# Kernel optimization log

Hardware: AMD Instinct MI355X
Metric: run time of the kernel (lower is better)

## Reference

```python
import jax, jax.numpy as jnp
import numpy as np
import math

N_HEAD = 16
N_KV_HEAD = 4
WINDOW = 512
EPS = 1e-6


def _rotate_half(t):
    t1, t2 = jnp.split(t, 2, axis=-1)
    return jnp.concatenate([-t2, t1], axis=-1)


def _rope_tables(T, head_dim):
    theta = 1.0 / (10000.0 ** (jnp.arange(0, head_dim, 2, dtype=jnp.float32) / head_dim))
    pos = jnp.arange(T, dtype=jnp.float32)
    freqs = jnp.outer(pos, theta)                      # [T, d/2]
    cos = jnp.concatenate([jnp.cos(freqs), jnp.cos(freqs)], axis=-1)  # [T, d]
    sin = jnp.concatenate([jnp.sin(freqs), jnp.sin(freqs)], axis=-1)
    return cos, sin


def setup_inputs() -> dict:
    key = jax.random.key(0)
    k1, k2, k3, k4 = jax.random.split(key, 4)
    B, T, C = 1, 2048, 1024
    kv_out = 2 * N_KV_HEAD * (C // N_HEAD)  # 512
    x = jax.random.normal(k1, (B, T, C), dtype=jnp.float32)
    Wq = jax.random.normal(k2, (C, C), dtype=jnp.float32) * 0.02
    Wkv = jax.random.normal(k3, (kv_out, C), dtype=jnp.float32) * 0.02
    Wproj = jax.random.normal(k4, (C, C), dtype=jnp.float32) * 0.02
    return {"x": x, "Wq": Wq, "Wkv": Wkv, "Wproj": Wproj}


def reference(x, Wq, Wkv, Wproj):
    B, T, C = x.shape
    H, KV = N_HEAD, N_KV_HEAD
    d = C // H
    n_rep = H // KV

    q = (x @ Wq.T).reshape(B, T, H, d).transpose(0, 2, 1, 3)     # [B,H,T,d]
    kv = x @ Wkv.T                                               # [B,T,2*KV*d]
    k, v = jnp.split(kv, 2, axis=2)
    k = k.reshape(B, T, KV, d).transpose(0, 2, 1, 3)             # [B,KV,T,d]
    v = v.reshape(B, T, KV, d).transpose(0, 2, 1, 3)

    # QK L2 normalization
    q = q / (jnp.linalg.norm(q, axis=-1, keepdims=True) + EPS)
    k = k / (jnp.linalg.norm(k, axis=-1, keepdims=True) + EPS)

    # RoPE
    cos, sin = _rope_tables(T, d)
    cos = cos[None, None]  # [1,1,T,d]
    sin = sin[None, None]
    q = q * cos + _rotate_half(q) * sin
    k = k * cos + _rotate_half(k) * sin

    # GQA: repeat KV heads (repeat_interleave on head dim)
    k = jnp.repeat(k, n_rep, axis=1)   # [B,H,T,d]
    v = jnp.repeat(v, n_rep, axis=1)

    # sliding-window causal mask: cols <= rows and cols > rows - WINDOW
    rows = jnp.arange(T)[:, None]
    cols = jnp.arange(T)[None, :]
    mask = (cols <= rows) & (cols > rows - WINDOW)  # [T,T] bool

    scale = 1.0 / math.sqrt(d)
    scores = jnp.einsum("bhqd,bhkd->bhqk", q, k) * scale
    scores = jnp.where(mask[None, None], scores, -jnp.inf)
    attn = jax.nn.softmax(scores, axis=-1)
    y = jnp.einsum("bhqk,bhkd->bhqd", attn, v)      # [B,H,T,d]
    y = y.transpose(0, 2, 1, 3).reshape(B, T, C)
    return y @ Wproj.T
```

## Files before the change

kernel.cpp:

```cpp
#include <hip/hip_runtime.h>

#define T_SEQ 2048
#define C_DIM 1024
#define NH    16
#define NKV   4
#define HD    64
#define WIN   512

typedef __bf16 bf16x8 __attribute__((ext_vector_type(8)));
typedef __bf16 bf16x4 __attribute__((ext_vector_type(4)));
typedef float f32x4 __attribute__((ext_vector_type(4)));

#define MFMA16(a, b, c) __builtin_amdgcn_mfma_f32_16x16x32_bf16(a, b, c, 0, 0, 0)

__global__ __launch_bounds__(256) void prep_kernel(const float* __restrict__ x,
                                                   const float* __restrict__ Wq,
                                                   const float* __restrict__ Wkv,
                                                   const float* __restrict__ Wp,
                                                   __bf16* __restrict__ xb,
                                                   __bf16* __restrict__ Wqkvb,
                                                   __bf16* __restrict__ Wpb,
                                                   float2* __restrict__ ropeT) {
  int b = blockIdx.x;
  if (b >= 4608) {
    int idx = (b - 4608) * 256 + threadIdx.x;
    int t = idx >> 5, i = idx & 31;
    float theta = exp2f(-(float)i * (13.287712379549449f / 32.0f));
    float s, c;
    sincosf((float)t * theta, &s, &c);
    ropeT[idx] = make_float2(c, s);
    return;
  }
  const float* src;
  __bf16* dst;
  int off;
  if (b < 2048)      { src = x;   dst = xb;                off = b; }
  else if (b < 3072) { src = Wq;  dst = Wqkvb;             off = b - 2048; }
  else if (b < 3584) { src = Wkv; dst = Wqkvb + (1 << 20); off = b - 3072; }
  else               { src = Wp;  dst = Wpb;               off = b - 3584; }
  int i = off * 1024 + threadIdx.x * 4;
  float4 v = *(const float4*)(src + i);
  bf16x4 o;
  o[0] = (__bf16)v.x; o[1] = (__bf16)v.y; o[2] = (__bf16)v.z; o[3] = (__bf16)v.w;
  *(bf16x4*)(dst + i) = o;
}

__device__ __forceinline__ void gemm_core64(const __bf16* __restrict__ A,
                                            const __bf16* __restrict__ B,
                                            int K,
                                            __bf16* AsB, __bf16* BsB,
                                            f32x4 (&acc)[4]) {
  const int tid = threadIdx.x;
  const int w = tid >> 6, l = tid & 63;
  const int quad = l >> 4, r16 = l & 15;
  const int srow = tid >> 2;
  const int sc0  = (tid & 3) * 2;
  const int wS0 = srow * 64 + ((sc0 ^ (srow & 7)) * 8);
  const int wS1 = srow * 64 + (((sc0 + 1) ^ (srow & 7)) * 8);
  const __bf16* gA = A + (size_t)srow * K + sc0 * 8;
  const __bf16* gB = B + (size_t)srow * K + sc0 * 8;
  int rA[2], rB[4][2];
#pragma unroll
  for (int ks = 0; ks < 2; ++ks) {
    int row = w * 16 + r16;
    rA[ks] = row * 64 + (((ks * 4 + quad) ^ (row & 7)) * 8);
  }
#pragma unroll
  for (int nt = 0; nt < 4; ++nt)
#pragma unroll
    for (int ks = 0; ks < 2; ++ks) {
      int row = nt * 16 + r16;
      rB[nt][ks] = row * 64 + (((ks * 4 + quad) ^ (row & 7)) * 8);
    }
  const int nIter = K >> 6;
  uint4 a0, a1, b0, b1;
  { const uint4* p = (const uint4*)gA; a0 = p[0]; a1 = p[1]; }
  { const uint4* p = (const uint4*)gB; b0 = p[0]; b1 = p[1]; }
  *(uint4*)(AsB + wS0) = a0; *(uint4*)(AsB + wS1) = a1;
  *(uint4*)(BsB + wS0) = b0; *(uint4*)(BsB + wS1) = b1;
  __syncthreads();
  int cur = 0;
  for (int it = 0; it < nIter; ++it) {
    if (it + 1 < nIter) {
      const uint4* p = (const uint4*)(gA + ((it + 1) << 6));
      a0 = p[0]; a1 = p[1];
      const uint4* q = (const uint4*)(gB + ((it + 1) << 6));
      b0 = q[0]; b1 = q[1];
    }
    const __bf16* Asc = AsB + cur * 4096;
    const __bf16* Bsc = BsB + cur * 4096;
#pragma unroll
    for (int ks = 0; ks < 2; ++ks) {
      bf16x8 fa  = *(const bf16x8*)(Asc + rA[ks]);
      bf16x8 fb0 = *(const bf16x8*)(Bsc + rB[0][ks]);
      bf16x8 fb1 = *(const bf16x8*)(Bsc + rB[1][ks]);
      bf16x8 fb2 = *(const bf16x8*)(Bsc + rB[2][ks]);
      bf16x8 fb3 = *(const bf16x8*)(Bsc + rB[3][ks]);
      acc[0] = MFMA16(fa, fb0, acc[0]);
      acc[1] = MFMA16(fa, fb1, acc[1]);
      acc[2] = MFMA16(fa, fb2, acc[2]);
      acc[3] = MFMA16(fa, fb3, acc[3]);
    }
    if (it + 1 < nIter) {
      __builtin_amdgcn_sched_barrier(0);
      __bf16* Asn = AsB + (cur ^ 1) * 4096;
      __bf16* Bsn = BsB + (cur ^ 1) * 4096;
      *(uint4*)(Asn + wS0) = a0; *(uint4*)(Asn + wS1) = a1;
      *(uint4*)(Bsn + wS0) = b0; *(uint4*)(Bsn + wS1) = b1;
      __syncthreads();
      cur ^= 1;
    }
  }
}

__global__ __launch_bounds__(256) void gemm_qkv_kernel(const __bf16* __restrict__ xb,
                                                       const __bf16* __restrict__ Wqkvb,
                                                       const float2* __restrict__ ropeT,
                                                       __bf16* __restrict__ Qb,
                                                       __bf16* __restrict__ Kb,
                                                       __bf16* __restrict__ Vt) {
  __shared__ __align__(16) __bf16 smem[16384];
  __bf16* AsB = smem;
  __bf16* BsB = smem + 8192;
  f32x4 acc[4] = {};
  const int m0 = blockIdx.y * 64, n0 = blockIdx.x * 64;
  gemm_core64(xb + (size_t)m0 * C_DIM, Wqkvb + (size_t)n0 * C_DIM, C_DIM, AsB, BsB, acc);
  const int tid = threadIdx.x;
  const int w = tid >> 6, l = tid & 63, quad = l >> 4, r16 = l & 15;
  if (n0 < 1280) {
    const bool isQ = n0 < 1024;
    const int head = isQ ? (n0 >> 6) : ((n0 - 1024) >> 6);
    __bf16* dstBase = (isQ ? Qb : Kb) + (size_t)head * T_SEQ * HD;
    const float osc = isQ ? 0.125f : 1.0f;
#pragma unroll
    for (int r = 0; r < 4; ++r) {
      float ss = acc[0][r] * acc[0][r] + acc[1][r] * acc[1][r] +
                 acc[2][r] * acc[2][r] + acc[3][r] * acc[3][r];
#pragma unroll
      for (int m = 1; m < 16; m <<= 1) ss += __shfl_xor(ss, m, 64);
      const float inv = osc / (sqrtf(ss) + 1e-6f);
      const int t = m0 + w * 16 + quad * 4 + r;
      const float2 cs0 = ropeT[t * 32 + r16];
      const float2 cs1 = ropeT[t * 32 + 16 + r16];
      const float v0 = acc[0][r] * inv, v1 = acc[1][r] * inv;
      const float v2 = acc[2][r] * inv, v3 = acc[3][r] * inv;
      __bf16* dst = dstBase + (size_t)t * HD;
      dst[r16]      = (__bf16)(v0 * cs0.x - v2 * cs0.y);
      dst[16 + r16] = (__bf16)(v1 * cs1.x - v3 * cs1.y);
      dst[32 + r16] = (__bf16)(v2 * cs0.x + v0 * cs0.y);
      dst[48 + r16] = (__bf16)(v3 * cs1.x + v1 * cs1.y);
    }
  } else {
    const int kvh = (n0 - 1280) >> 6;
    __syncthreads();
    __bf16* Vs = smem;
#pragma unroll
    for (int nt = 0; nt < 4; ++nt)
#pragma unroll
      for (int r = 0; r < 4; ++r)
        Vs[(nt * 16 + r16) * 136 + w * 16 + quad * 4 + r] = (__bf16)acc[nt][r];
    __syncthreads();
    const int d = tid >> 2, tc = (tid & 3) * 16;
    __bf16* dst = Vt + ((size_t)kvh * HD + d) * T_SEQ + m0 + tc;
    bf16x8 v0 = *(const bf16x8*)(Vs + d * 136 + tc);
    bf16x8 v1 = *(const bf16x8*)(Vs + d * 136 + tc + 8);
    *(bf16x8*)dst = v0;
    *(bf16x8*)(dst + 8) = v1;
  }
}

__global__ __launch_bounds__(256) void gemm_proj_kernel(const __bf16* __restrict__ Yb,
                                                        const __bf16* __restrict__ Wpb,
                                                        float* __restrict__ C) {
  __shared__ __align__(16) __bf16 smem[16384];
  __bf16* AsB = smem;
  __bf16* BsB = smem + 8192;
  f32x4 acc[4] = {};
  const int m0 = blockIdx.y * 64, n0 = blockIdx.x * 64;
  gemm_core64(Yb + (size_t)m0 * C_DIM, Wpb + (size_t)n0 * C_DIM, C_DIM, AsB, BsB, acc);
  const int tid = threadIdx.x;
  const int w = tid >> 6, l = tid & 63, quad = l >> 4, r16 = l & 15;
  const int mrow = m0 + w * 16 + quad * 4;
  const int ncol = n0 + r16;
#pragma unroll
  for (int r = 0; r < 4; ++r) {
    size_t rowoff = (size_t)(mrow + r) * C_DIM;
    C[rowoff + ncol]      = acc[0][r];
    C[rowoff + ncol + 16] = acc[1][r];
    C[rowoff + ncol + 32] = acc[2][r];
    C[rowoff + ncol + 48] = acc[3][r];
  }
}

__global__ __launch_bounds__(256) void attn_mfma_kernel(const __bf16* __restrict__ Qb,
                                                        const __bf16* __restrict__ Kb,
                                                        const __bf16* __restrict__ Vt,
                                                        __bf16* __restrict__ Yb) {
  __shared__ __align__(16) __bf16 Pl[4][16][72];
  __shared__ __align__(16) float Oc[2][16][68];
  __shared__ float Ls[2][16];
  const int h = blockIdx.y, kvh = h >> 2;
  const int t0 = blockIdx.x * 32;
  const int tid = threadIdx.x;
  const int w = tid >> 6, l = tid & 63;
  const int quad = l >> 4, r16 = l & 15;
  const int sub = w & 1, half = w >> 1;
  const __bf16* qptr = Qb + ((size_t)h * T_SEQ + t0 + sub * 16 + r16) * HD + quad * 8;
  bf16x8 aq0 = *(const bf16x8*)(qptr);
  bf16x8 aq1 = *(const bf16x8*)(qptr + 32);
  const int keyStart = max(0, t0 - (WIN - 1)) & ~63;
  const int keyEnd = (t0 + 32 + 63) & ~63;
  const int nch = (keyEnd - keyStart) >> 6;
  const int nch2 = (nch + 1) >> 1;
  const int cbeg = half ? nch2 : 0;
  const int cend = half ? nch : nch2;
  const __bf16* kbase = Kb + (size_t)kvh * T_SEQ * HD;
  const __bf16* vbase = Vt + (size_t)kvh * HD * T_SEQ;
  const int tq_base = t0 + sub * 16 + quad * 4;
  f32x4 oacc[4] = {};
  float lsum[4] = {0.f, 0.f, 0.f, 0.f};
  for (int c = cbeg; c < cend; ++c) {
    const int key0 = keyStart + (c << 6);
    f32x4 s[4] = {};
#pragma unroll
    for (int nt = 0; nt < 4; ++nt) {
      const __bf16* kr = kbase + (size_t)(key0 + nt * 16 + r16) * HD + quad * 8;
      bf16x8 bk0 = *(const bf16x8*)kr;
      bf16x8 bk1 = *(const bf16x8*)(kr + 32);
      s[nt] = MFMA16(aq0, bk0, s[nt]);
      s[nt] = MFMA16(aq1, bk1, s[nt]);
    }
#pragma unroll
    for (int nt = 0; nt < 4; ++nt) {
      const int key = key0 + nt * 16 + r16;
#pragma unroll
      for (int r = 0; r < 4; ++r) {
        const int tq = tq_base + r;
        bool valid = (key <= tq) && (key > tq - WIN);
        float p = valid ? __expf(s[nt][r]) : 0.0f;
        lsum[r] += p;
        Pl[w][quad * 4 + r][nt * 16 + r16] = (__bf16)p;
      }
    }
    bf16x8 ap0 = *(const bf16x8*)(&Pl[w][r16][quad * 8]);
    bf16x8 ap1 = *(const bf16x8*)(&Pl[w][r16][32 + quad * 8]);
#pragma unroll
    for (int nt = 0; nt < 4; ++nt) {
      const __bf16* vr = vbase + (size_t)(nt * 16 + r16) * T_SEQ + key0 + quad * 8;
      bf16x8 bv0 = *(const bf16x8*)vr;
      bf16x8 bv1 = *(const bf16x8*)(vr + 32);
      oacc[nt] = MFMA16(ap0, bv0, oacc[nt]);
      oacc[nt] = MFMA16(ap1, bv1, oacc[nt]);
    }
  }
#pragma unroll
  for (int r = 0; r < 4; ++r) {
#pragma unroll
    for (int m = 1; m < 16; m <<= 1) lsum[r] += __shfl_xor(lsum[r], m, 64);
  }
  if (half == 1) {
#pragma unroll
    for (int nt = 0; nt < 4; ++nt)
#pragma unroll
      for (int r = 0; r < 4; ++r)
        Oc[sub][quad * 4 + r][nt * 16 + r16] = oacc[nt][r];
    if (r16 == 0) {
#pragma unroll
      for (int r = 0; r < 4; ++r) Ls[sub][quad * 4 + r] = lsum[r];
    }
  }
  __syncthreads();
  if (half == 0) {
#pragma unroll
    for (int r = 0; r < 4; ++r) {
      const float inv = 1.0f / (lsum[r] + Ls[sub][quad * 4 + r]);
      const size_t row = (size_t)(tq_base + r);
#pragma unroll
      for (int nt = 0; nt < 4; ++nt) {
        float o = oacc[nt][r] + Oc[sub][quad * 4 + r][nt * 16 + r16];
        Yb[row * C_DIM + h * HD + nt * 16 + r16] = (__bf16)(o * inv);
      }
    }
  }
}

extern "C" void kernel_launch(void* const* d_in, const int* in_sizes, int n_in,
                              void* d_out, int out_size, void* d_ws, size_t ws_size,
                              hipStream_t stream) {
  const float* x     = (const float*)d_in[0];
  const float* Wq    = (const float*)d_in[1];
  const float* Wkv   = (const float*)d_in[2];
  const float* Wproj = (const float*)d_in[3];
  float* out = (float*)d_out;

  __bf16* xb    = (__bf16*)d_ws;
  __bf16* Wqkvb = xb + (size_t)T_SEQ * C_DIM;
  __bf16* Wpb   = Wqkvb + (size_t)1536 * C_DIM;
  __bf16* Qb    = Wpb + (size_t)C_DIM * C_DIM;
  __bf16* Kb    = Qb + (size_t)NH * T_SEQ * HD;
  __bf16* Vt    = Kb + (size_t)NKV * T_SEQ * HD;
  __bf16* Yb    = Vt + (size_t)NKV * HD * T_SEQ;
  float2* ropeT = (float2*)(Yb + (size_t)T_SEQ * C_DIM);

  prep_kernel<<<4864, 256, 0, stream>>>(x, Wq, Wkv, Wproj, xb, Wqkvb, Wpb, ropeT);
  gemm_qkv_kernel<<<dim3(24, 32), 256, 0, stream>>>(xb, Wqkvb, ropeT, Qb, Kb, Vt);
  attn_mfma_kernel<<<dim3(T_SEQ / 32, NH), 256, 0, stream>>>(Qb, Kb, Vt, Yb);
  gemm_proj_kernel<<<dim3(16, 32), 256, 0, stream>>>(Yb, Wpb, out);
}
```

Baseline: 133.1 us.

## Split K across two thread groups in both GEMMs with shared-memory reduction

Both GEMM kernels now launch 512 threads per block. Each 256-thread half computes the 64x64 tile over half of the K dimension, using its own double-buffered shared-memory region. The second half writes its partial accumulators to shared memory and the first half adds them before the epilogue. This aims to double the waves per tile and improve latency hiding for small grids (768 and 512 blocks). The cost is twice the shared memory per block, an extra reduction round, and idle threads during the epilogue.

New measurement: 135.4 us. About the same (+1.7%).

```diff
diff --git a/kernel.cpp b/kernel.cpp
--- a/kernel.cpp
+++ b/kernel.cpp
@@ -45,20 +45,25 @@
   *(bf16x4*)(dst + i) = o;
 }
 
-__device__ __forceinline__ void gemm_core64(const __bf16* __restrict__ A,
-                                            const __bf16* __restrict__ B,
-                                            int K,
-                                            __bf16* AsB, __bf16* BsB,
-                                            f32x4 (&acc)[4]) {
-  const int tid = threadIdx.x;
+__device__ __forceinline__ void gemm_core_sk(const __bf16* __restrict__ A,
+                                             const __bf16* __restrict__ B,
+                                             int K,
+                                             __bf16* smem,
+                                             f32x4 (&acc)[4]) {
+  const int tid512 = threadIdx.x;
+  const int g = tid512 >> 8;
+  const int tid = tid512 & 255;
   const int w = tid >> 6, l = tid & 63;
   const int quad = l >> 4, r16 = l & 15;
   const int srow = tid >> 2;
   const int sc0  = (tid & 3) * 2;
   const int wS0 = srow * 64 + ((sc0 ^ (srow & 7)) * 8);
   const int wS1 = srow * 64 + (((sc0 + 1) ^ (srow & 7)) * 8);
-  const __bf16* gA = A + (size_t)srow * K + sc0 * 8;
-  const __bf16* gB = B + (size_t)srow * K + sc0 * 8;
+  const int kOff = g * (K >> 1);
+  const __bf16* gA = A + (size_t)srow * K + kOff + sc0 * 8;
+  const __bf16* gB = B + (size_t)srow * K + kOff + sc0 * 8;
+  __bf16* AsB = smem + g * 16384;
+  __bf16* BsB = smem + g * 16384 + 8192;
   int rA[2], rB[4][2];
 #pragma unroll
   for (int ks = 0; ks < 2; ++ks) {
@@ -72,7 +77,7 @@
       int row = nt * 16 + r16;
       rB[nt][ks] = row * 64 + (((ks * 4 + quad) ^ (row & 7)) * 8);
     }
-  const int nIter = K >> 6;
+  const int nIter = (K >> 1) >> 6;
   uint4 a0, a1, b0, b1;
   { const uint4* p = (const uint4*)gA; a0 = p[0]; a1 = p[1]; }
   { const uint4* p = (const uint4*)gB; b0 = p[0]; b1 = p[1]; }
@@ -111,74 +116,95 @@
       cur ^= 1;
     }
   }
-}
-
-__global__ __launch_bounds__(256) void gemm_qkv_kernel(const __bf16* __restrict__ xb,
-                                                       const __bf16* __restrict__ Wqkvb,
-                                                       const float2* __restrict__ ropeT,
-                                                       __bf16* __restrict__ Qb,
-                                                       __bf16* __restrict__ Kb,
-                                                       __bf16* __restrict__ Vt) {
-  __shared__ __align__(16) __bf16 smem[16384];
-  __bf16* AsB = smem;
-  __bf16* BsB = smem + 8192;
+  __syncthreads();
+  float* Sc = (float*)smem;
+  if (g == 1) {
+#pragma unroll
+    for (int nt = 0; nt < 4; ++nt)
+      *(f32x4*)(Sc + (nt * 16 + r16) * 68 + (w * 16 + quad * 4)) = acc[nt];
+  }
+  __syncthreads();
+  if (g == 0) {
+#pragma unroll
+    for (int nt = 0; nt < 4; ++nt) {
+      f32x4 o = *(const f32x4*)(Sc + (nt * 16 + r16) * 68 + (w * 16 + quad * 4));
+      acc[nt] = acc[nt] + o;
+    }
+  }
+}
+
+__global__ __launch_bounds__(512, 4) void gemm_qkv_kernel(const __bf16* __restrict__ xb,
+                                                          const __bf16* __restrict__ Wqkvb,
+                                                          const float2* __restrict__ ropeT,
+                                                          __bf16* __restrict__ Qb,
+                                                          __bf16* __restrict__ Kb,
+                                                          __bf16* __restrict__ Vt) {
+  __shared__ __align__(16) __bf16 smem[32768];
   f32x4 acc[4] = {};
   const int m0 = blockIdx.y * 64, n0 = blockIdx.x * 64;
-  gemm_core64(xb + (size_t)m0 * C_DIM, Wqkvb + (size_t)n0 * C_DIM, C_DIM, AsB, BsB, acc);
-  const int tid = threadIdx.x;
+  gemm_core_sk(xb + (size_t)m0 * C_DIM, Wqkvb + (size_t)n0 * C_DIM, C_DIM, smem, acc);
+  const int tid512 = threadIdx.x;
+  const int g = tid512 >> 8;
+  const int tid = tid512 & 255;
   const int w = tid >> 6, l = tid & 63, quad = l >> 4, r16 = l & 15;
   if (n0 < 1280) {
-    const bool isQ = n0 < 1024;
-    const int head = isQ ? (n0 >> 6) : ((n0 - 1024) >> 6);
-    __bf16* dstBase = (isQ ? Qb : Kb) + (size_t)head * T_SEQ * HD;
-    const float osc = isQ ? 0.125f : 1.0f;
-#pragma unroll
-    for (int r = 0; r < 4; ++r) {
-      float ss = acc[0][r] * acc[0][r] + acc[1][r] * acc[1][r] +
-                 acc[2][r] * acc[2][r] + acc[3][r] * acc[3][r];
-#pragma unroll
-      for (int m = 1; m < 16; m <<= 1) ss += __shfl_xor(ss, m, 64);
-      const float inv = osc / (sqrtf(ss) + 1e-6f);
-      const int t = m0 + w * 16 + quad * 4 + r;
-      const float2 cs0 = ropeT[t * 32 + r16];
-      const float2 cs1 = ropeT[t * 32 + 16 + r16];
-      const float v0 = acc[0][r] * inv, v1 = acc[1][r] * inv;
-      const float v2 = acc[2][r] * inv, v3 = acc[3][r] * inv;
-      __bf16* dst = dstBase + (size_t)t * HD;
-      dst[r16]      = (__bf16)(v0 * cs0.x - v2 * cs0.y);
-      dst[16 + r16] = (__bf16)(v1 * cs1.x - v3 * cs1.y);
-      dst[32 + r16] = (__bf16)(v2 * cs0.x + v0 * cs0.y);
-      dst[48 + r16] = (__bf16)(v3 * cs1.x + v1 * cs1.y);
+    if (g == 0) {
+      const bool isQ = n0 < 1024;
+      const int head = isQ ? (n0 >> 6) : ((n0 - 1024) >> 6);
+      __bf16* dstBase = (isQ ? Qb : Kb) + (size_t)head * T_SEQ * HD;
+      const float osc = isQ ? 0.125f : 1.0f;
+#pragma unroll
+      for (int r = 0; r < 4; ++r) {
+        float ss = acc[0][r] * acc[0][r] + acc[1][r] * acc[1][r] +
+                   acc[2][r] * acc[2][r] + acc[3][r] * acc[3][r];
+#pragma unroll
+        for (int m = 1; m < 16; m <<= 1) ss += __shfl_xor(ss, m, 64);
+        const float inv = osc / (sqrtf(ss) + 1e-6f);
+        const int t = m0 + w * 16 + quad * 4 + r;
+        const float2 cs0 = ropeT[t * 32 + r16];
+        const float2 cs1 = ropeT[t * 32 + 16 + r16];
+        const float v0 = acc[0][r] * inv, v1 = acc[1][r] * inv;
+        const float v2 = acc[2][r] * inv, v3 = acc[3][r] * inv;
+        __bf16* dst = dstBase + (size_t)t * HD;
+        dst[r16]      = (__bf16)(v0 * cs0.x - v2 * cs0.y);
+        dst[16 + r16] = (__bf16)(v1 * cs1.x - v3 * cs1.y);
+        dst[32 + r16] = (__bf16)(v2 * cs0.x + v0 * cs0.y);
+        dst[48 + r16] = (__bf16)(v3 * cs1.x + v1 * cs1.y);
+      }
     }
   } else {
     const int kvh = (n0 - 1280) >> 6;
     __syncthreads();
     __bf16* Vs = smem;
-#pragma unroll
-    for (int nt = 0; nt < 4; ++nt)
-#pragma unroll
-      for (int r = 0; r < 4; ++r)
-        Vs[(nt * 16 + r16) * 136 + w * 16 + quad * 4 + r] = (__bf16)acc[nt][r];
+    if (g == 0) {
+#pragma unroll
+      for (int nt = 0; nt < 4; ++nt)
+#pragma unroll
+        for (int r = 0; r < 4; ++r)
+          Vs[(nt * 16 + r16) * 136 + w * 16 + quad * 4 + r] = (__bf16)acc[nt][r];
+    }
     __syncthreads();
-    const int d = tid >> 2, tc = (tid & 3) * 16;
-    __bf16* dst = Vt + ((size_t)kvh * HD + d) * T_SEQ + m0 + tc;
-    bf16x8 v0 = *(const bf16x8*)(Vs + d * 136 + tc);
-    bf16x8 v1 = *(const bf16x8*)(Vs + d * 136 + tc + 8);
-    *(bf16x8*)dst = v0;
-    *(bf16x8*)(dst + 8) = v1;
-  }
-}
-
-__global__ __launch_bounds__(256) void gemm_proj_kernel(const __bf16* __restrict__ Yb,
-                                                        const __bf16* __restrict__ Wpb,
-                                                        float* __restrict__ C) {
-  __shared__ __align__(16) __bf16 smem[16384];
-  __bf16* AsB = smem;
-  __bf16* BsB = smem + 8192;
+    if (g == 0) {
+      const int d = tid >> 2, tc = (tid & 3) * 16;
+      __bf16* dst = Vt + ((size_t)kvh * HD + d) * T_SEQ + m0 + tc;
+      bf16x8 v0 = *(const bf16x8*)(Vs + d * 136 + tc);
+      bf16x8 v1 = *(const bf16x8*)(Vs + d * 136 + tc + 8);
+      *(bf16x8*)dst = v0;
+      *(bf16x8*)(dst + 8) = v1;
+    }
+  }
+}
+
+__global__ __launch_bounds__(512, 4) void gemm_proj_kernel(const __bf16* __restrict__ Yb,
+                                                           const __bf16* __restrict__ Wpb,
+                                                           float* __restrict__ C) {
+  __shared__ __align__(16) __bf16 smem[32768];
   f32x4 acc[4] = {};
   const int m0 = blockIdx.y * 64, n0 = blockIdx.x * 64;
-  gemm_core64(Yb + (size_t)m0 * C_DIM, Wpb + (size_t)n0 * C_DIM, C_DIM, AsB, BsB, acc);
-  const int tid = threadIdx.x;
+  gemm_core_sk(Yb + (size_t)m0 * C_DIM, Wpb + (size_t)n0 * C_DIM, C_DIM, smem, acc);
+  const int tid512 = threadIdx.x;
+  if (tid512 >= 256) return;
+  const int tid = tid512;
   const int w = tid >> 6, l = tid & 63, quad = l >> 4, r16 = l & 15;
   const int mrow = m0 + w * 16 + quad * 4;
   const int ncol = n0 + r16;
@@ -303,7 +329,7 @@
   float2* ropeT = (float2*)(Yb + (size_t)T_SEQ * C_DIM);
 
   prep_kernel<<<4864, 256, 0, stream>>>(x, Wq, Wkv, Wproj, xb, Wqkvb, Wpb, ropeT);
-  gemm_qkv_kernel<<<dim3(24, 32), 256, 0, stream>>>(xb, Wqkvb, ropeT, Qb, Kb, Vt);
+  gemm_qkv_kernel<<<dim3(24, 32), 512, 0, stream>>>(xb, Wqkvb, ropeT, Qb, Kb, Vt);
   attn_mfma_kernel<<<dim3(T_SEQ / 32, NH), 256, 0, stream>>>(Qb, Kb, Vt, Yb);
-  gemm_proj_kernel<<<dim3(16, 32), 256, 0, stream>>>(Yb, Wpb, out);
-}
+  gemm_proj_kernel<<<dim3(16, 32), 512, 0, stream>>>(Yb, Wpb, out);
+}
```

## Fuse all four stages into one persistent kernel with grid barriers

Applied to the files above, without the earlier changes.

Replaces the four separate launches (prep, QKV GEMM, attention, projection GEMM) with a single persistent kernel of 1024 blocks that runs each stage in turn, separated by atomic-counter grid barriers. The barrier counters are cleared with a memset before launch. The aim is to remove the launch gaps and tail effects between kernels. In exchange, the spin-wait barriers cost time, some blocks sit idle in the GEMM stages, and the scheme only works if all 1024 blocks are resident at once (launch_bounds 256,4). If they are not, it deadlocks.

Result: slower. 468.0 us (+251.6%).

```diff
diff --git a/kernel.cpp b/kernel.cpp
--- a/kernel.cpp
+++ b/kernel.cpp
@@ -6,6 +6,7 @@
 #define NKV   4
 #define HD    64
 #define WIN   512
+#define NBLK  1024u
 
 typedef __bf16 bf16x8 __attribute__((ext_vector_type(8)));
 typedef __bf16 bf16x4 __attribute__((ext_vector_type(4)));
@@ -13,36 +14,15 @@
 
 #define MFMA16(a, b, c) __builtin_amdgcn_mfma_f32_16x16x32_bf16(a, b, c, 0, 0, 0)
 
-__global__ __launch_bounds__(256) void prep_kernel(const float* __restrict__ x,
-                                                   const float* __restrict__ Wq,
-                                                   const float* __restrict__ Wkv,
-                                                   const float* __restrict__ Wp,
-                                                   __bf16* __restrict__ xb,
-                                                   __bf16* __restrict__ Wqkvb,
-                                                   __bf16* __restrict__ Wpb,
-                                                   float2* __restrict__ ropeT) {
-  int b = blockIdx.x;
-  if (b >= 4608) {
-    int idx = (b - 4608) * 256 + threadIdx.x;
-    int t = idx >> 5, i = idx & 31;
-    float theta = exp2f(-(float)i * (13.287712379549449f / 32.0f));
-    float s, c;
-    sincosf((float)t * theta, &s, &c);
-    ropeT[idx] = make_float2(c, s);
-    return;
-  }
-  const float* src;
-  __bf16* dst;
-  int off;
-  if (b < 2048)      { src = x;   dst = xb;                off = b; }
-  else if (b < 3072) { src = Wq;  dst = Wqkvb;             off = b - 2048; }
-  else if (b < 3584) { src = Wkv; dst = Wqkvb + (1 << 20); off = b - 3072; }
-  else               { src = Wp;  dst = Wpb;               off = b - 3584; }
-  int i = off * 1024 + threadIdx.x * 4;
-  float4 v = *(const float4*)(src + i);
-  bf16x4 o;
-  o[0] = (__bf16)v.x; o[1] = (__bf16)v.y; o[2] = (__bf16)v.z; o[3] = (__bf16)v.w;
-  *(bf16x4*)(dst + i) = o;
+__device__ __forceinline__ void grid_barrier(unsigned* cnt) {
+  __syncthreads();
+  if (threadIdx.x == 0) {
+    __threadfence();
+    atomicAdd(cnt, 1u);
+    while (atomicAdd(cnt, 0u) < NBLK) __builtin_amdgcn_s_sleep(8);
+    __threadfence();
+  }
+  __syncthreads();
 }
 
 __device__ __forceinline__ void gemm_core64(const __bf16* __restrict__ A,
@@ -113,173 +93,199 @@
   }
 }
 
-__global__ __launch_bounds__(256) void gemm_qkv_kernel(const __bf16* __restrict__ xb,
-                                                       const __bf16* __restrict__ Wqkvb,
-                                                       const float2* __restrict__ ropeT,
+__global__ __launch_bounds__(256, 4) void fused_kernel(const float* __restrict__ x,
+                                                       const float* __restrict__ Wq,
+                                                       const float* __restrict__ Wkv,
+                                                       const float* __restrict__ Wp,
+                                                       __bf16* __restrict__ xb,
+                                                       __bf16* __restrict__ Wqkvb,
+                                                       __bf16* __restrict__ Wpb,
+                                                       float2* __restrict__ ropeT,
                                                        __bf16* __restrict__ Qb,
                                                        __bf16* __restrict__ Kb,
-                                                       __bf16* __restrict__ Vt) {
+                                                       __bf16* __restrict__ Vt,
+                                                       __bf16* __restrict__ Yb,
+                                                       float* __restrict__ out,
+                                                       unsigned* __restrict__ bar) {
   __shared__ __align__(16) __bf16 smem[16384];
-  __bf16* AsB = smem;
-  __bf16* BsB = smem + 8192;
-  f32x4 acc[4] = {};
-  const int m0 = blockIdx.y * 64, n0 = blockIdx.x * 64;
-  gemm_core64(xb + (size_t)m0 * C_DIM, Wqkvb + (size_t)n0 * C_DIM, C_DIM, AsB, BsB, acc);
+  const int bid = blockIdx.x;
   const int tid = threadIdx.x;
   const int w = tid >> 6, l = tid & 63, quad = l >> 4, r16 = l & 15;
-  if (n0 < 1280) {
-    const bool isQ = n0 < 1024;
-    const int head = isQ ? (n0 >> 6) : ((n0 - 1024) >> 6);
-    __bf16* dstBase = (isQ ? Qb : Kb) + (size_t)head * T_SEQ * HD;
-    const float osc = isQ ? 0.125f : 1.0f;
+
+  for (int b = bid; b < 4864; b += (int)NBLK) {
+    if (b >= 4608) {
+      int idx = (b - 4608) * 256 + tid;
+      int t = idx >> 5, i = idx & 31;
+      float theta = exp2f(-(float)i * (13.287712379549449f / 32.0f));
+      float s, c;
+      sincosf((float)t * theta, &s, &c);
+      ropeT[idx] = make_float2(c, s);
+    } else {
+      const float* src;
+      __bf16* dst;
+      int off;
+      if (b < 2048)      { src = x;   dst = xb;                off = b; }
+      else if (b < 3072) { src = Wq;  dst = Wqkvb;             off = b - 2048; }
+      else if (b < 3584) { src = Wkv; dst = Wqkvb + (1 << 20); off = b - 3072; }
+      else               { src = Wp;  dst = Wpb;               off = b - 3584; }
+      int i = off * 1024 + tid * 4;
+      float4 v = *(const float4*)(src + i);
+      bf16x4 o;
+      o[0] = (__bf16)v.x; o[1] = (__bf16)v.y; o[2] = (__bf16)v.z; o[3] = (__bf16)v.w;
+      *(bf16x4*)(dst + i) = o;
+    }
+  }
+  grid_barrier(bar + 0);
+
+  if (bid < 768) {
+    f32x4 acc[4] = {};
+    const int m0 = (bid / 24) * 64, n0 = (bid % 24) * 64;
+    gemm_core64(xb + (size_t)m0 * C_DIM, Wqkvb + (size_t)n0 * C_DIM, C_DIM,
+                smem, smem + 8192, acc);
+    if (n0 < 1280) {
+      const bool isQ = n0 < 1024;
+      const int head = isQ ? (n0 >> 6) : ((n0 - 1024) >> 6);
+      __bf16* dstBase = (isQ ? Qb : Kb) + (size_t)head * T_SEQ * HD;
+      const float osc = isQ ? 0.125f : 1.0f;
+#pragma unroll
+      for (int r = 0; r < 4; ++r) {
+        float ss = acc[0][r] * acc[0][r] + acc[1][r] * acc[1][r] +
+                   acc[2][r] * acc[2][r] + acc[3][r] * acc[3][r];
+#pragma unroll
+        for (int m = 1; m < 16; m <<= 1) ss += __shfl_xor(ss, m, 64);
+        const float inv = osc / (sqrtf(ss) + 1e-6f);
+        const int t = m0 + w * 16 + quad * 4 + r;
+        const float2 cs0 = ropeT[t * 32 + r16];
+        const float2 cs1 = ropeT[t * 32 + 16 + r16];
+        const float v0 = acc[0][r] * inv, v1 = acc[1][r] * inv;
+        const float v2 = acc[2][r] * inv, v3 = acc[3][r] * inv;
+        __bf16* dst = dstBase + (size_t)t * HD;
+        dst[r16]      = (__bf16)(v0 * cs0.x - v2 * cs0.y);
+        dst[16 + r16] = (__bf16)(v1 * cs1.x - v3 * cs1.y);
+        dst[32 + r16] = (__bf16)(v2 * cs0.x + v0 * cs0.y);
+        dst[48 + r16] = (__bf16)(v3 * cs1.x + v1 * cs1.y);
+      }
+    } else {
+      const int kvh = (n0 - 1280) >> 6;
+      __syncthreads();
+      __bf16* Vs = smem;
+#pragma unroll
+      for (int nt = 0; nt < 4; ++nt)
+#pragma unroll
+        for (int r = 0; r < 4; ++r)
+          Vs[(nt * 16 + r16) * 136 + w * 16 + quad * 4 + r] = (__bf16)acc[nt][r];
+      __syncthreads();
+      const int d = tid >> 2, tc = (tid & 3) * 16;
+      __bf16* dst = Vt + ((size_t)kvh * HD + d) * T_SEQ + m0 + tc;
+      bf16x8 v0 = *(const bf16x8*)(Vs + d * 136 + tc);
+      bf16x8 v1 = *(const bf16x8*)(Vs + d * 136 + tc + 8);
+      *(bf16x8*)dst = v0;
+      *(bf16x8*)(dst + 8) = v1;
+    }
+  }
+  grid_barrier(bar + 1);
+
+  {
+    __bf16* Pl = smem;
+    float*  Oc = (float*)(smem + 4608);
+    float*  Ls = Oc + 2176;
+    const int h = bid >> 6, kvh = h >> 2;
+    const int t0 = (bid & 63) * 32;
+    const int sub = w & 1, half = w >> 1;
+    const __bf16* qptr = Qb + ((size_t)h * T_SEQ + t0 + sub * 16 + r16) * HD + quad * 8;
+    bf16x8 aq0 = *(const bf16x8*)(qptr);
+    bf16x8 aq1 = *(const bf16x8*)(qptr + 32);
+    const int keyStart = max(0, t0 - (WIN - 1)) & ~63;
+    const int keyEnd = (t0 + 32 + 63) & ~63;
+    const int nch = (keyEnd - keyStart) >> 6;
+    const int nch2 = (nch + 1) >> 1;
+    const int cbeg = half ? nch2 : 0;
+    const int cend = half ? nch : nch2;
+    const __bf16* kbase = Kb + (size_t)kvh * T_SEQ * HD;
+    const __bf16* vbase = Vt + (size_t)kvh * HD * T_SEQ;
+    const int tq_base = t0 + sub * 16 + quad * 4;
+    f32x4 oacc[4] = {};
+    float lsum[4] = {0.f, 0.f, 0.f, 0.f};
+    for (int c = cbeg; c < cend; ++c) {
+      const int key0 = keyStart + (c << 6);
+      f32x4 s[4] = {};
+#pragma unroll
+      for (int nt = 0; nt < 4; ++nt) {
+        const __bf16* kr = kbase + (size_t)(key0 + nt * 16 + r16) * HD + quad * 8;
+        bf16x8 bk0 = *(const bf16x8*)kr;
+        bf16x8 bk1 = *(const bf16x8*)(kr + 32);
+        s[nt] = MFMA16(aq0, bk0, s[nt]);
+        s[nt] = MFMA16(aq1, bk1, s[nt]);
+      }
+#pragma unroll
+      for (int nt = 0; nt < 4; ++nt) {
+        const int key = key0 + nt * 16 + r16;
+#pragma unroll
+        for (int r = 0; r < 4; ++r) {
+          const int tq = tq_base + r;
+          bool valid = (key <= tq) && (key > tq - WIN);
+          float p = valid ? __expf(s[nt][r]) : 0.0f;
+          lsum[r] += p;
+          Pl[(w * 16 + quad * 4 + r) * 72 + nt * 16 + r16] = (__bf16)p;
+        }
+      }
+      bf16x8 ap0 = *(const bf16x8*)(Pl + (w * 16 + r16) * 72 + quad * 8);
+      bf16x8 ap1 = *(const bf16x8*)(Pl + (w * 16 + r16) * 72 + 32 + quad * 8);
+#pragma unroll
+      for (int nt = 0; nt < 4; ++nt) {
+        const __bf16* vr = vbase + (size_t)(nt * 16 + r16) * T_SEQ + key0 + quad * 8;
+        bf16x8 bv0 = *(const bf16x8*)vr;
+        bf16x8 bv1 = *(const bf16x8*)(vr + 32);
+        oacc[nt] = MFMA16(ap0, bv0, oacc[nt]);
+        oacc[nt] = MFMA16(ap1, bv1, oacc[nt]);
+      }
+    }
 #pragma unroll
     for (int r = 0; r < 4; ++r) {
-      float ss = acc[0][r] * acc[0][r] + acc[1][r] * acc[1][r] +
-                 acc[2][r] * acc[2][r] + acc[3][r] * acc[3][r];
-#pragma unroll
-      for (int m = 1; m < 16; m <<= 1) ss += __shfl_xor(ss, m, 64);
-      const float inv = osc / (sqrtf(ss) + 1e-6f);
-      const int t = m0 + w * 16 + quad * 4 + r;
-      const float2 cs0 = ropeT[t * 32 + r16];
-      const float2 cs1 = ropeT[t * 32 + 16 + r16];
-      const float v0 = acc[0][r] * inv, v1 = acc[1][r] * inv;
-      const float v2 = acc[2][r] * inv, v3 = acc[3][r] * inv;
-      __bf16* dst = dstBase + (size_t)t * HD;
-      dst[r16]      = (__bf16)(v0 * cs0.x - v2 * cs0.y);
-      dst[16 + r16] = (__bf16)(v1 * cs1.x - v3 * cs1.y);
-      dst[32 + r16] = (__bf16)(v2 * cs0.x + v0 * cs0.y);
-      dst[48 + r16] = (__bf16)(v3 * cs1.x + v1 * cs1.y);
-    }
-  } else {
-    const int kvh = (n0 - 1280) >> 6;
+#pragma unroll
+      for (int m = 1; m < 16; m <<= 1) lsum[r] += __shfl_xor(lsum[r], m, 64);
+    }
+    if (half == 1) {
+#pragma unroll
+      for (int nt = 0; nt < 4; ++nt)
+#pragma unroll
+        for (int r = 0; r < 4; ++r)
+          Oc[(sub * 16 + quad * 4 + r) * 68 + nt * 16 + r16] = oacc[nt][r];
+      if (r16 == 0) {
+#pragma unroll
+        for (int r = 0; r < 4; ++r) Ls[sub * 16 + quad * 4 + r] = lsum[r];
+      }
+    }
     __syncthreads();
-    __bf16* Vs = smem;
-#pragma unroll
-    for (int nt = 0; nt < 4; ++nt)
-#pragma unroll
-      for (int r = 0; r < 4; ++r)
-        Vs[(nt * 16 + r16) * 136 + w * 16 + quad * 4 + r] = (__bf16)acc[nt][r];
-    __syncthreads();
-    const int d = tid >> 2, tc = (tid & 3) * 16;
-    __bf16* dst = Vt + ((size_t)kvh * HD + d) * T_SEQ + m0 + tc;
-    bf16x8 v0 = *(const bf16x8*)(Vs + d * 136 + tc);
-    bf16x8 v1 = *(const bf16x8*)(Vs + d * 136 + tc + 8);
-    *(bf16x8*)dst = v0;
-    *(bf16x8*)(dst + 8) = v1;
-  }
-}
-
-__global__ __launch_bounds__(256) void gemm_proj_kernel(const __bf16* __restrict__ Yb,
-                                                        const __bf16* __restrict__ Wpb,
-                                                        float* __restrict__ C) {
-  __shared__ __align__(16) __bf16 smem[16384];
-  __bf16* AsB = smem;
-  __bf16* BsB = smem + 8192;
-  f32x4 acc[4] = {};
-  const int m0 = blockIdx.y * 64, n0 = blockIdx.x * 64;
-  gemm_core64(Yb + (size_t)m0 * C_DIM, Wpb + (size_t)n0 * C_DIM, C_DIM, AsB, BsB, acc);
-  const int tid = threadIdx.x;
-  const int w = tid >> 6, l = tid & 63, quad = l >> 4, r16 = l & 15;
-  const int mrow = m0 + w * 16 + quad * 4;
-  const int ncol = n0 + r16;
-#pragma unroll
-  for (int r = 0; r < 4; ++r) {
-    size_t rowoff = (size_t)(mrow + r) * C_DIM;
-    C[rowoff + ncol]      = acc[0][r];
-    C[rowoff + ncol + 16] = acc[1][r];
-    C[rowoff + ncol + 32] = acc[2][r];
-    C[rowoff + ncol + 48] = acc[3][r];
-  }
-}
-
-__global__ __launch_bounds__(256) void attn_mfma_kernel(const __bf16* __restrict__ Qb,
-                                                        const __bf16* __restrict__ Kb,
-                                                        const __bf16* __restrict__ Vt,
-                                                        __bf16* __restrict__ Yb) {
-  __shared__ __align__(16) __bf16 Pl[4][16][72];
-  __shared__ __align__(16) float Oc[2][16][68];
-  __shared__ float Ls[2][16];
-  const int h = blockIdx.y, kvh = h >> 2;
-  const int t0 = blockIdx.x * 32;
-  const int tid = threadIdx.x;
-  const int w = tid >> 6, l = tid & 63;
-  const int quad = l >> 4, r16 = l & 15;
-  const int sub = w & 1, half = w >> 1;
-  const __bf16* qptr = Qb + ((size_t)h * T_SEQ + t0 + sub * 16 + r16) * HD + quad * 8;
-  bf16x8 aq0 = *(const bf16x8*)(qptr);
-  bf16x8 aq1 = *(const bf16x8*)(qptr + 32);
-  const int keyStart = max(0, t0 - (WIN - 1)) & ~63;
-  const int keyEnd = (t0 + 32 + 63) & ~63;
-  const int nch = (keyEnd - keyStart) >> 6;
-  const int nch2 = (nch + 1) >> 1;
-  const int cbeg = half ? nch2 : 0;
-  const int cend = half ? nch : nch2;
-  const __bf16* kbase = Kb + (size_t)kvh * T_SEQ * HD;
-  const __bf16* vbase = Vt + (size_t)kvh * HD * T_SEQ;
-  const int tq_base = t0 + sub * 16 + quad * 4;
-  f32x4 oacc[4] = {};
-  float lsum[4] = {0.f, 0.f, 0.f, 0.f};
-  for (int c = cbeg; c < cend; ++c) {
-    const int key0 = keyStart + (c << 6);
-    f32x4 s[4] = {};
-#pragma unroll
-    for (int nt = 0; nt < 4; ++nt) {
-      const __bf16* kr = kbase + (size_t)(key0 + nt * 16 + r16) * HD + quad * 8;
-      bf16x8 bk0 = *(const bf16x8*)kr;
-      bf16x8 bk1 = *(const bf16x8*)(kr + 32);
-      s[nt] = MFMA16(aq0, bk0, s[nt]);
-      s[nt] = MFMA16(aq1, bk1, s[nt]);
-    }
-#pragma unroll
-    for (int nt = 0; nt < 4; ++nt) {
-      const int key = key0 + nt * 16 + r16;
+    if (half == 0) {
 #pragma unroll
       for (int r = 0; r < 4; ++r) {
-        const int tq = tq_base + r;
-        bool valid = (key <= tq) && (key > tq - WIN);
-        float p = valid ? __expf(s[nt][r]) : 0.0f;
-        lsum[r] += p;
-        Pl[w][quad * 4 + r][nt * 16 + r16] = (__bf16)p;
-      }
-    }
-    bf16x8 ap0 = *(const bf16x8*)(&Pl[w][r16][quad * 8]);
-    bf16x8 ap1 = *(const bf16x8*)(&Pl[w][r16][32 + quad * 8]);
-#pragma unroll
-    for (int nt = 0; nt < 4; ++nt) {
-      const __bf16* vr = vbase + (size_t)(nt * 16 + r16) * T_SEQ + key0 + quad * 8;
-      bf16x8 bv0 = *(const bf16x8*)vr;
-      bf16x8 bv1 = *(const bf16x8*)(vr + 32);
-      oacc[nt] = MFMA16(ap0, bv0, oacc[nt]);
-      oacc[nt] = MFMA16(ap1, bv1, oacc[nt]);
-    }
-  }
-#pragma unroll
-  for (int r = 0; r < 4; ++r) {
-#pragma unroll
-    for (int m = 1; m < 16; m <<= 1) lsum[r] += __shfl_xor(lsum[r], m, 64);
-  }
-  if (half == 1) {
-#pragma unroll
-    for (int nt = 0; nt < 4; ++nt)
-#pragma unroll
-      for (int r = 0; r < 4; ++r)
-        Oc[sub][quad * 4 + r][nt * 16 + r16] = oacc[nt][r];
-    if (r16 == 0) {
-#pragma unroll
-      for (int r = 0; r < 4; ++r) Ls[sub][quad * 4 + r] = lsum[r];
-    }
-  }
-  __syncthreads();
-  if (half == 0) {
+        const float inv = 1.0f / (lsum[r] + Ls[sub * 16 + quad * 4 + r]);
+        const size_t row = (size_t)(tq_base + r);
+#pragma unroll
+        for (int nt = 0; nt < 4; ++nt) {
+          float o = oacc[nt][r] + Oc[(sub * 16 + quad * 4 + r) * 68 + nt * 16 + r16];
+          Yb[row * C_DIM + h * HD + nt * 16 + r16] = (__bf16)(o * inv);
+        }
+      }
+    }
+  }
+  grid_barrier(bar + 2);
+
+  if (bid < 512) {
+    f32x4 acc[4] = {};
+    const int m0 = (bid >> 4) * 64, n0 = (bid & 15) * 64;
+    gemm_core64(Yb + (size_t)m0 * C_DIM, Wpb + (size_t)n0 * C_DIM, C_DIM,
+                smem, smem + 8192, acc);
+    const int mrow = m0 + w * 16 + quad * 4;
+    const int ncol = n0 + r16;
 #pragma unroll
     for (int r = 0; r < 4; ++r) {
-      const float inv = 1.0f / (lsum[r] + Ls[sub][quad * 4 + r]);
-      const size_t row = (size_t)(tq_base + r);
-#pragma unroll
-      for (int nt = 0; nt < 4; ++nt) {
-        float o = oacc[nt][r] + Oc[sub][quad * 4 + r][nt * 16 + r16];
-        Yb[row * C_DIM + h * HD + nt * 16 + r16] = (__bf16)(o * inv);
-      }
+      size_t rowoff = (size_t)(mrow + r) * C_DIM;
+      out[rowoff + ncol]      = acc[0][r];
+      out[rowoff + ncol + 16] = acc[1][r];
+      out[rowoff + ncol + 32] = acc[2][r];
+      out[rowoff + ncol + 48] = acc[3][r];
     }
   }
 }
@@ -293,17 +299,17 @@
   const float* Wproj = (const float*)d_in[3];
   float* out = (float*)d_out;
 
-  __bf16* xb    = (__bf16*)d_ws;
-  __bf16* Wqkvb = xb + (size_t)T_SEQ * C_DIM;
-  __bf16* Wpb   = Wqkvb + (size_t)1536 * C_DIM;
-  __bf16* Qb    = Wpb + (size_t)C_DIM * C_DIM;
-  __bf16* Kb    = Qb + (size_t)NH * T_SEQ * HD;
-  __bf16* Vt    = Kb + (size_t)NKV * T_SEQ * HD;
-  __bf16* Yb    = Vt + (size_t)NKV * HD * T_SEQ;
-  float2* ropeT = (float2*)(Yb + (size_t)T_SEQ * C_DIM);
-
-  prep_kernel<<<4864, 256, 0, stream>>>(x, Wq, Wkv, Wproj, xb, Wqkvb, Wpb, ropeT);
-  gemm_qkv_kernel<<<dim3(24, 32), 256, 0, stream>>>(xb, Wqkvb, ropeT, Qb, Kb, Vt);
-  attn_mfma_kernel<<<dim3(T_SEQ / 32, NH), 256, 0, stream>>>(Qb, Kb, Vt, Yb);
-  gemm_proj_kernel<<<dim3(16, 32), 256, 0, stream>>>(Yb, Wpb, out);
+  __bf16*   xb    = (__bf16*)d_ws;
+  __bf16*   Wqkvb = xb + (size_t)T_SEQ * C_DIM;
+  __bf16*   Wpb   = Wqkvb + (size_t)1536 * C_DIM;
+  __bf16*   Qb    = Wpb + (size_t)C_DIM * C_DIM;
+  __bf16*   Kb    = Qb + (size_t)NH * T_SEQ * HD;
+  __bf16*   Vt    = Kb + (size_t)NKV * T_SEQ * HD;
+  __bf16*   Yb    = Vt + (size_t)NKV * HD * T_SEQ;
+  float2*   ropeT = (float2*)(Yb + (size_t)T_SEQ * C_DIM);
+  unsigned* bar   = (unsigned*)(ropeT + 2048 * 32);
+
+  hipMemsetAsync(bar, 0, 64, stream);
+  fused_kernel<<<NBLK, 256, 0, stream>>>(x, Wq, Wkv, Wproj, xb, Wqkvb, Wpb, ropeT,
+                                         Qb, Kb, Vt, Yb, out, bar);
 }
```

## Split attention key range across four waves per 16-query block

Applied to the files above, without the earlier changes.

Each attention block now handles 16 queries instead of 32, and the key chunks are split four ways across the waves rather than two ways per query subtile. Partial outputs and row sums from all four waves are reduced through shared memory, which is also reused as the P staging buffer. This doubles the grid size for better occupancy and load balance. The cost is that each K/V chunk is loaded for fewer queries, so global traffic goes up, and there is an extra sync and reduction step.

Result: slower. 136.8 us (+2.8%).

```diff
diff --git a/kernel.cpp b/kernel.cpp
--- a/kernel.cpp
+++ b/kernel.cpp
@@ -196,27 +196,25 @@
                                                         const __bf16* __restrict__ Kb,
                                                         const __bf16* __restrict__ Vt,
                                                         __bf16* __restrict__ Yb) {
-  __shared__ __align__(16) __bf16 Pl[4][16][72];
-  __shared__ __align__(16) float Oc[2][16][68];
-  __shared__ float Ls[2][16];
+  __shared__ __align__(16) float Oc[4][16][68];
+  __shared__ float Ls[4][16];
   const int h = blockIdx.y, kvh = h >> 2;
-  const int t0 = blockIdx.x * 32;
+  const int t0 = blockIdx.x * 16;
   const int tid = threadIdx.x;
   const int w = tid >> 6, l = tid & 63;
   const int quad = l >> 4, r16 = l & 15;
-  const int sub = w & 1, half = w >> 1;
-  const __bf16* qptr = Qb + ((size_t)h * T_SEQ + t0 + sub * 16 + r16) * HD + quad * 8;
+  __bf16* Plw = ((__bf16*)&Oc[0][0][0]) + w * 1152;
+  const __bf16* qptr = Qb + ((size_t)h * T_SEQ + t0 + r16) * HD + quad * 8;
   bf16x8 aq0 = *(const bf16x8*)(qptr);
   bf16x8 aq1 = *(const bf16x8*)(qptr + 32);
   const int keyStart = max(0, t0 - (WIN - 1)) & ~63;
-  const int keyEnd = (t0 + 32 + 63) & ~63;
+  const int keyEnd = (t0 + 16 + 63) & ~63;
   const int nch = (keyEnd - keyStart) >> 6;
-  const int nch2 = (nch + 1) >> 1;
-  const int cbeg = half ? nch2 : 0;
-  const int cend = half ? nch : nch2;
+  const int cbeg = (w * nch) >> 2;
+  const int cend = ((w + 1) * nch) >> 2;
   const __bf16* kbase = Kb + (size_t)kvh * T_SEQ * HD;
   const __bf16* vbase = Vt + (size_t)kvh * HD * T_SEQ;
-  const int tq_base = t0 + sub * 16 + quad * 4;
+  const int tq_base = t0 + quad * 4;
   f32x4 oacc[4] = {};
   float lsum[4] = {0.f, 0.f, 0.f, 0.f};
   for (int c = cbeg; c < cend; ++c) {
@@ -239,11 +237,11 @@
         bool valid = (key <= tq) && (key > tq - WIN);
         float p = valid ? __expf(s[nt][r]) : 0.0f;
         lsum[r] += p;
-        Pl[w][quad * 4 + r][nt * 16 + r16] = (__bf16)p;
+        Plw[(quad * 4 + r) * 72 + nt * 16 + r16] = (__bf16)p;
       }
     }
-    bf16x8 ap0 = *(const bf16x8*)(&Pl[w][r16][quad * 8]);
-    bf16x8 ap1 = *(const bf16x8*)(&Pl[w][r16][32 + quad * 8]);
+    bf16x8 ap0 = *(const bf16x8*)(Plw + r16 * 72 + quad * 8);
+    bf16x8 ap1 = *(const bf16x8*)(Plw + r16 * 72 + 32 + quad * 8);
 #pragma unroll
     for (int nt = 0; nt < 4; ++nt) {
       const __bf16* vr = vbase + (size_t)(nt * 16 + r16) * T_SEQ + key0 + quad * 8;
@@ -258,28 +256,26 @@
 #pragma unroll
     for (int m = 1; m < 16; m <<= 1) lsum[r] += __shfl_xor(lsum[r], m, 64);
   }
-  if (half == 1) {
-#pragma unroll
-    for (int nt = 0; nt < 4; ++nt)
-#pragma unroll
-      for (int r = 0; r < 4; ++r)
-        Oc[sub][quad * 4 + r][nt * 16 + r16] = oacc[nt][r];
-    if (r16 == 0) {
-#pragma unroll
-      for (int r = 0; r < 4; ++r) Ls[sub][quad * 4 + r] = lsum[r];
-    }
-  }
   __syncthreads();
-  if (half == 0) {
-#pragma unroll
-    for (int r = 0; r < 4; ++r) {
-      const float inv = 1.0f / (lsum[r] + Ls[sub][quad * 4 + r]);
-      const size_t row = (size_t)(tq_base + r);
-#pragma unroll
-      for (int nt = 0; nt < 4; ++nt) {
-        float o = oacc[nt][r] + Oc[sub][quad * 4 + r][nt * 16 + r16];
-        Yb[row * C_DIM + h * HD + nt * 16 + r16] = (__bf16)(o * inv);
-      }
+#pragma unroll
+  for (int nt = 0; nt < 4; ++nt)
+#pragma unroll
+    for (int r = 0; r < 4; ++r)
+      Oc[w][quad * 4 + r][nt * 16 + r16] = oacc[nt][r];
+  if (r16 == 0) {
+#pragma unroll
+    for (int r = 0; r < 4; ++r) Ls[w][quad * 4 + r] = lsum[r];
+  }
+  __syncthreads();
+  {
+    const int col = tid & 63;
+    const int r0 = tid >> 6;
+#pragma unroll
+    for (int rr = 0; rr < 4; ++rr) {
+      const int row = r0 + rr * 4;
+      float o = Oc[0][row][col] + Oc[1][row][col] + Oc[2][row][col] + Oc[3][row][col];
+      float dl = Ls[0][row] + Ls[1][row] + Ls[2][row] + Ls[3][row];
+      Yb[(size_t)(t0 + row) * C_DIM + h * HD + col] = (__bf16)(o / dl);
     }
   }
 }
@@ -304,6 +300,6 @@
 
   prep_kernel<<<4864, 256, 0, stream>>>(x, Wq, Wkv, Wproj, xb, Wqkvb, Wpb, ropeT);
   gemm_qkv_kernel<<<dim3(24, 32), 256, 0, stream>>>(xb, Wqkvb, ropeT, Qb, Kb, Vt);
-  attn_mfma_kernel<<<dim3(T_SEQ / 32, NH), 256, 0, stream>>>(Qb, Kb, Vt, Yb);
+  attn_mfma_kernel<<<dim3(T_SEQ / 16, NH), 256, 0, stream>>>(Qb, Kb, Vt, Yb);
   gemm_proj_kernel<<<dim3(16, 32), 256, 0, stream>>>(Yb, Wpb, out);
 }
```
